# Optimization experiments

Measured on AMD Instinct MI355X. Metric: run time of the kernel, lower is better.

## Reference

```python
import jax, jax.numpy as jnp
import numpy as np

NEG_SLOPE = 0.2  # PyG GATConv default LeakyReLU slope


def _gat_conv(x, edge_index, W, a_src, a_dst, bias, heads, out_dim, concat):
    """PyG-style GATConv (eval mode, add_self_loops=True).
    x: [N, F_in], edge_index: [2, E] (row=src, col=dst)."""
    N = x.shape[0]
    loops = jnp.tile(jnp.arange(N, dtype=edge_index.dtype)[None, :], (2, 1))
    ei = jnp.concatenate([edge_index, loops], axis=1)  # [2, E+N]
    src, dst = ei[0], ei[1]

    h = (x @ W).reshape(N, heads, out_dim)            # [N, H, D]
    alpha_s = jnp.einsum('nhd,hd->nh', h, a_src)       # [N, H]
    alpha_d = jnp.einsum('nhd,hd->nh', h, a_dst)       # [N, H]

    e = jax.nn.leaky_relu(alpha_s[src] + alpha_d[dst], NEG_SLOPE)  # [E', H]
    # segment softmax over edges grouped by destination node
    m = jax.ops.segment_max(e, dst, num_segments=N)
    e = jnp.exp(e - jax.lax.stop_gradient(m)[dst])
    denom = jax.ops.segment_sum(e, dst, num_segments=N)
    alpha = e / denom[dst]                              # [E', H]

    msg = h[src] * alpha[..., None]                     # [E', H, D]
    out = jax.ops.segment_sum(msg, dst, num_segments=N) # [N, H, D]
    out = out.reshape(N, heads * out_dim) if concat else out.mean(axis=1)
    return out + bias


def setup_inputs() -> dict:
    key = jax.random.key(0)
    ks = jax.random.split(key, 12)
    N, E, F_in, H, D = 50000, 1600000, 64, 2, 32
    s = 0.1
    return {
        'x': jax.random.normal(ks[0], (N, F_in), jnp.float32),
        'edge_index': jax.random.randint(ks[1], (2, E), 0, N, jnp.int64 if jax.config.jax_enable_x64 else jnp.int32),
        'W1': jax.random.normal(ks[2], (F_in, H * D), jnp.float32) * s,
        'a_src1': jax.random.normal(ks[3], (H, D), jnp.float32) * s,
        'a_dst1': jax.random.normal(ks[4], (H, D), jnp.float32) * s,
        'b1': jnp.zeros((H * D,), jnp.float32),
        'W2': jax.random.normal(ks[5], (H * D, D), jnp.float32) * s,
        'a_src2': jax.random.normal(ks[6], (1, D), jnp.float32) * s,
        'a_dst2': jax.random.normal(ks[7], (1, D), jnp.float32) * s,
        'b2': jnp.zeros((D,), jnp.float32),
        'fcW': jax.random.normal(ks[8], (D, 1), jnp.float32) * s,
        'fcb': jnp.zeros((1,), jnp.float32),
    }


def reference(x, edge_index, W1, a_src1, a_dst1, b1, W2, a_src2, a_dst2, b2, fcW, fcb):
    H, D = 2, 32
    h = _gat_conv(x, edge_index, W1, a_src1, a_dst1, b1, heads=H, out_dim=D, concat=True)
    h = jax.nn.elu(h)
    # dropout p=0.1 is a no-op in eval mode
    h = _gat_conv(h, edge_index, W2, a_src2, a_dst2, b2, heads=1, out_dim=D, concat=False)
    h = jax.nn.elu(h)
    scores = h @ fcW + fcb
    return (scores, h)
```

## Files before the change

kernel.cpp:

```cpp
#include <hip/hip_runtime.h>
#include <hip/hip_fp16.h>

#define NEG_SLOPE 0.2f
#define NRANGE 4
#define ILV 13
#define CAP 96

__device__ __forceinline__ float elu_f(float x) {
    return x > 0.f ? x : __expf(x) - 1.f;
}
__device__ __forceinline__ float lrelu_f(float x) {
    return fmaxf(x, NEG_SLOPE * x);
}

union H4 { float2 f2; __half2 h2[2]; };

__global__ __launch_bounds__(256) void scat_gemm1_kernel(
    const int* __restrict__ ei, int* __restrict__ cnt,
    unsigned short* __restrict__ srclist, int E, int N,
    int nScat, int nChunks,
    const float* __restrict__ x, const float* __restrict__ W1,
    const float* __restrict__ a_src, const float* __restrict__ a_dst,
    __half* __restrict__ h1, float* __restrict__ as1, float* __restrict__ ad1)
{
    __shared__ float Xl[4][64];
    int b = blockIdx.x;
    if (b < ILV * nScat && (b % ILV) == 0) {
        int hid = b / ILV;
        int range = hid & (NRANGE - 1);
        int chunk = hid >> 2;
        int RS = (N + NRANGE - 1) / NRANGE;
        int lo = range * RS;
        unsigned span = (unsigned)(((lo + RS) > N ? N : (lo + RS)) - lo);
        int per = (((E + nChunks - 1) / nChunks) + 7) & ~7;
        int beg = chunk * per;
        int end = beg + per; if (end > E) end = E;
        if (beg >= E) return;

        int nfull = (end - beg) >> 11;
        for (int j = 0; j < nfull; ++j) {
            int i = beg + (j << 11) + (int)threadIdx.x * 8;
            int4 d0 = *(const int4*)(ei + E + i);
            int4 d1 = *(const int4*)(ei + E + i + 4);
            int4 s0 = *(const int4*)(ei + i);
            int4 s1 = *(const int4*)(ei + i + 4);
            int ds[8] = { d0.x, d0.y, d0.z, d0.w, d1.x, d1.y, d1.z, d1.w };
            int ss[8] = { s0.x, s0.y, s0.z, s0.w, s1.x, s1.y, s1.z, s1.w };
            int pos[8];
            bool pr[8];
#pragma unroll
            for (int k = 0; k < 8; ++k) {
                pr[k] = (unsigned)(ds[k] - lo) < span;
                if (pr[k]) pos[k] = atomicAdd(&cnt[ds[k]], 1);
            }
#pragma unroll
            for (int k = 0; k < 8; ++k) {
                if (pr[k])
                    srclist[(size_t)ds[k] * CAP + pos[k]] =
                        (unsigned short)ss[k];
            }
        }
        for (int i = beg + (nfull << 11) + (int)threadIdx.x; i < end; i += 256) {
            int dst = ei[E + i];
            if ((unsigned)(dst - lo) < span) {
                int src = ei[i];
                int pos = atomicAdd(&cnt[dst], 1);
                srclist[(size_t)dst * CAP + pos] = (unsigned short)src;
            }
        }
        return;
    }
    int gid = (b < ILV * nScat) ? (b - b / ILV - 1) : (b - nScat);
    int tid = threadIdx.x;
    int r   = tid >> 6;
    int col = tid & 63;
    int row = gid * 4 + r;
    if (row < N) Xl[r][col] = x[(size_t)row * 64 + col];
    __syncthreads();
    if (row >= N) return;

    float acc = 0.f;
#pragma unroll
    for (int k = 0; k < 64; ++k) acc += Xl[r][k] * W1[k * 64 + col];
    h1[(size_t)row * 64 + col] = __float2half(acc);

    int head = col >> 5;
    float ps = acc * a_src[col];
    float pd = acc * a_dst[col];
#pragma unroll
    for (int off = 16; off; off >>= 1) {
        ps += __shfl_xor(ps, off, 32);
        pd += __shfl_xor(pd, off, 32);
    }
    if ((col & 31) == 0) {
        as1[row * 2 + head] = ps;
        ad1[row * 2 + head] = pd;
    }
}

__global__ __launch_bounds__(256) void agg1_gemm2_kernel(
    const int* __restrict__ dcnt, const unsigned short* __restrict__ srclist,
    const __half* __restrict__ h1, const float* __restrict__ as1,
    const float* __restrict__ ad1, const float* __restrict__ b1,
    const float* __restrict__ W2, const float* __restrict__ a_s2,
    const float* __restrict__ a_d2,
    __half* __restrict__ h2, float* __restrict__ as2, float* __restrict__ ad2,
    int N)
{
    __shared__ float W2l[64 * 32];
    __shared__ float sh[4][64];
    int tid = threadIdx.x;
    for (int i = tid; i < 64 * 32; i += 256) W2l[i] = W2[i];
    __syncthreads();

    int n = (blockIdx.x * 256 + tid) >> 6;
    int lane = tid & 63;
    int wid = tid >> 6;
    if (n >= N) return;

    int grp = lane >> 4;
    int cl  = lane & 15;
    int head = cl >> 3;
    const __half* h1q = h1 + 4 * cl;
    float2 adp = *(const float2*)(ad1 + (size_t)n * 2);

    float den0 = 0.f, den1 = 0.f;
    float a0 = 0.f, a1 = 0.f, a2 = 0.f, a3 = 0.f;
    int beg = n * CAP;
    int deg = dcnt[n];
    int total = deg + 1;

    for (int base = 0; base < total; base += 64) {
        int li = base + lane;
        int es = (li < deg) ? (int)srclist[beg + li] : n;
        float2 asp = *(const float2*)(as1 + (size_t)es * 2);
        float w0 = 0.f, w1 = 0.f;
        if (li < total) {
            w0 = __expf(lrelu_f(asp.x + adp.x));
            w1 = __expf(lrelu_f(asp.y + adp.y));
        }
        den0 += w0; den1 += w1;

        int cnt = total - base; if (cnt > 64) cnt = 64;
        for (int j = 0; j < cnt; j += 16) {
            int e0 = j + grp, e1 = j + 4 + grp, e2 = j + 8 + grp, e3 = j + 12 + grp;
            int sA = __shfl(es, e0, 64);
            int sB = __shfl(es, e1, 64);
            int sC = __shfl(es, e2, 64);
            int sD = __shfl(es, e3, 64);
            float wA0 = __shfl(w0, e0, 64), wA1 = __shfl(w1, e0, 64);
            float wB0 = __shfl(w0, e1, 64), wB1 = __shfl(w1, e1, 64);
            float wC0 = __shfl(w0, e2, 64), wC1 = __shfl(w1, e2, 64);
            float wD0 = __shfl(w0, e3, 64), wD1 = __shfl(w1, e3, 64);
            float wA = head ? wA1 : wA0;
            float wB = head ? wB1 : wB0;
            float wC = head ? wC1 : wC0;
            float wD = head ? wD1 : wD0;
            H4 uA, uB, uC, uD;
            uA.f2 = *(const float2*)(h1q + (size_t)sA * 64);
            uB.f2 = *(const float2*)(h1q + (size_t)sB * 64);
            uC.f2 = *(const float2*)(h1q + (size_t)sC * 64);
            uD.f2 = *(const float2*)(h1q + (size_t)sD * 64);
            float2 gA01 = __half22float2(uA.h2[0]);
            float2 gA23 = __half22float2(uA.h2[1]);
            float2 gB01 = __half22float2(uB.h2[0]);
            float2 gB23 = __half22float2(uB.h2[1]);
            float2 gC01 = __half22float2(uC.h2[0]);
            float2 gC23 = __half22float2(uC.h2[1]);
            float2 gD01 = __half22float2(uD.h2[0]);
            float2 gD23 = __half22float2(uD.h2[1]);
            a0 += wA * gA01.x + wB * gB01.x + wC * gC01.x + wD * gD01.x;
            a1 += wA * gA01.y + wB * gB01.y + wC * gC01.y + wD * gD01.y;
            a2 += wA * gA23.x + wB * gB23.x + wC * gC23.x + wD * gD23.x;
            a3 += wA * gA23.y + wB * gB23.y + wC * gC23.y + wD * gD23.y;
        }
    }
    a0 += __shfl_xor(a0, 16, 64); a1 += __shfl_xor(a1, 16, 64);
    a2 += __shfl_xor(a2, 16, 64); a3 += __shfl_xor(a3, 16, 64);
    a0 += __shfl_xor(a0, 32, 64); a1 += __shfl_xor(a1, 32, 64);
    a2 += __shfl_xor(a2, 32, 64); a3 += __shfl_xor(a3, 32, 64);
#pragma unroll
    for (int off = 1; off < 64; off <<= 1) {
        den0 += __shfl_xor(den0, off, 64);
        den1 += __shfl_xor(den1, off, 64);
    }
    float den = head ? den1 : den0;

    float4 bb = *(const float4*)(b1 + 4 * cl);
    float inv = 1.f / den;
    float v0 = elu_f(a0 * inv + bb.x);
    float v1 = elu_f(a1 * inv + bb.y);
    float v2 = elu_f(a2 * inv + bb.z);
    float v3 = elu_f(a3 * inv + bb.w);
    if (grp == 0) ((float4*)sh[wid])[cl] = make_float4(v0, v1, v2, v3);

    int col = lane & 31;
    int kbase = (lane >> 5) * 32;
    float p = 0.f;
#pragma unroll
    for (int jj = 0; jj < 32; ++jj)
        p += sh[wid][kbase + jj] * W2l[(kbase + jj) * 32 + col];
    p += __shfl_xor(p, 32, 64);

    if (lane < 32) h2[(size_t)n * 32 + lane] = __float2half(p);

    float ps = p * a_s2[col];
    float pd = p * a_d2[col];
#pragma unroll
    for (int off = 16; off; off >>= 1) {
        ps += __shfl_xor(ps, off, 32);
        pd += __shfl_xor(pd, off, 32);
    }
    if (lane == 0) { as2[n] = ps; ad2[n] = pd; }
}

__global__ __launch_bounds__(256) void agg2_kernel(
    const int* __restrict__ dcnt, const unsigned short* __restrict__ srclist,
    const __half* __restrict__ h2, const float* __restrict__ as2,
    const float* __restrict__ ad2, const float* __restrict__ b2,
    const float* __restrict__ fcW, const float* __restrict__ fcb,
    float* __restrict__ out, int N)
{
    int g = blockIdx.x * 256 + threadIdx.x;
    int n = g >> 5;
    if (n >= N) return;
    int l32 = g & 31;
    int grp = l32 >> 3;
    int cl  = l32 & 7;
    float adn = ad2[n];
    const __half* h2q = h2 + 4 * cl;

    float denp = 0.f, a0 = 0.f, a1 = 0.f, a2 = 0.f, a3 = 0.f;
    int beg = n * CAP;
    int deg = dcnt[n];
    int total = deg + 1;

    for (int base = 0; base < total; base += 32) {
        int li = base + l32;
        int es = (li < deg) ? (int)srclist[beg + li] : n;
        float asv = as2[es];
        float w = 0.f;
        if (li < total) w = __expf(lrelu_f(asv + adn));
        denp += w;

        int cnt = total - base; if (cnt > 32) cnt = 32;
        for (int j = 0; j < cnt; j += 16) {
            int e0 = j + grp, e1 = j + 4 + grp, e2 = j + 8 + grp, e3 = j + 12 + grp;
            int sA = __shfl(es, e0, 32);
            int sB = __shfl(es, e1, 32);
            int sC = __shfl(es, e2, 32);
            int sD = __shfl(es, e3, 32);
            float wA = __shfl(w, e0, 32);
            float wB = __shfl(w, e1, 32);
            float wC = __shfl(w, e2, 32);
            float wD = __shfl(w, e3, 32);
            H4 uA, uB, uC, uD;
            uA.f2 = *(const float2*)(h2q + (size_t)sA * 32);
            uB.f2 = *(const float2*)(h2q + (size_t)sB * 32);
            uC.f2 = *(const float2*)(h2q + (size_t)sC * 32);
            uD.f2 = *(const float2*)(h2q + (size_t)sD * 32);
            float2 gA01 = __half22float2(uA.h2[0]);
            float2 gA23 = __half22float2(uA.h2[1]);
            float2 gB01 = __half22float2(uB.h2[0]);
            float2 gB23 = __half22float2(uB.h2[1]);
            float2 gC01 = __half22float2(uC.h2[0]);
            float2 gC23 = __half22float2(uC.h2[1]);
            float2 gD01 = __half22float2(uD.h2[0]);
            float2 gD23 = __half22float2(uD.h2[1]);
            a0 += wA * gA01.x + wB * gB01.x + wC * gC01.x + wD * gD01.x;
            a1 += wA * gA01.y + wB * gB01.y + wC * gC01.y + wD * gD01.y;
            a2 += wA * gA23.x + wB * gB23.x + wC * gC23.x + wD * gD23.x;
            a3 += wA * gA23.y + wB * gB23.y + wC * gC23.y + wD * gD23.y;
        }
    }
    a0 += __shfl_xor(a0, 8, 64);  a1 += __shfl_xor(a1, 8, 64);
    a2 += __shfl_xor(a2, 8, 64);  a3 += __shfl_xor(a3, 8, 64);
    a0 += __shfl_xor(a0, 16, 64); a1 += __shfl_xor(a1, 16, 64);
    a2 += __shfl_xor(a2, 16, 64); a3 += __shfl_xor(a3, 16, 64);
#pragma unroll
    for (int off = 1; off < 32; off <<= 1)
        denp += __shfl_xor(denp, off, 64);
    float den = denp;

    float4 bb = *(const float4*)(b2 + 4 * cl);
    float inv = 1.f / den;
    float v0 = elu_f(a0 * inv + bb.x);
    float v1 = elu_f(a1 * inv + bb.y);
    float v2 = elu_f(a2 * inv + bb.z);
    float v3 = elu_f(a3 * inv + bb.w);
    if (grp == 0)
        ((float4*)(out + (size_t)N + (size_t)n * 32))[cl] =
            make_float4(v0, v1, v2, v3);

    float4 fw = *(const float4*)(fcW + 4 * cl);
    float p = v0 * fw.x + v1 * fw.y + v2 * fw.z + v3 * fw.w;
    p += __shfl_xor(p, 1, 64);
    p += __shfl_xor(p, 2, 64);
    p += __shfl_xor(p, 4, 64);
    if (l32 == 0) out[n] = p + fcb[0];
}

extern "C" void kernel_launch(void* const* d_in, const int* in_sizes, int n_in,
                              void* d_out, int out_size, void* d_ws, size_t ws_size,
                              hipStream_t stream) {
    const float* x    = (const float*)d_in[0];
    const int*   ei   = (const int*)d_in[1];
    const float* W1   = (const float*)d_in[2];
    const float* a_s1 = (const float*)d_in[3];
    const float* a_d1 = (const float*)d_in[4];
    const float* b1   = (const float*)d_in[5];
    const float* W2   = (const float*)d_in[6];
    const float* a_s2 = (const float*)d_in[7];
    const float* a_d2 = (const float*)d_in[8];
    const float* b2   = (const float*)d_in[9];
    const float* fcW  = (const float*)d_in[10];
    const float* fcb  = (const float*)d_in[11];

    const int N = in_sizes[0] / 64;
    const int E = in_sizes[1] / 2;

    float* fws  = (float*)d_ws;
    float* as1  = fws;
    float* ad1  = as1 + (size_t)2 * N;
    float* as2  = ad1 + (size_t)2 * N;
    float* ad2  = as2 + (size_t)N;
    __half* h2  = (__half*)(ad2 + (size_t)N);
    __half* h1  = h2 + (size_t)32 * N;
    int*   cnt  = (int*)(h1 + (size_t)64 * N);
    unsigned short* srclist = (unsigned short*)(cnt + N);

    hipMemsetAsync(cnt, 0, sizeof(int) * (size_t)N, stream);

    const int nChunks = 256;
    const int nScat = nChunks * NRANGE;
    const int nG1 = (N + 3) / 4;
    int extra = nG1 - (ILV - 1) * nScat; if (extra < 0) extra = 0;
    scat_gemm1_kernel<<<ILV * nScat + extra, 256, 0, stream>>>(
        ei, cnt, srclist, E, N, nScat, nChunks, x, W1, a_s1, a_d1, h1, as1, ad1);

    agg1_gemm2_kernel<<<((size_t)N * 64 + 255) / 256, 256, 0, stream>>>(
        cnt, srclist, h1, as1, ad1, b1, W2, a_s2, a_d2, h2, as2, ad2, N);

    agg2_kernel<<<((size_t)N * 32 + 255) / 256, 256, 0, stream>>>(
        cnt, srclist, h2, as2, ad2, b2, fcW, fcb, (float*)d_out, N);
}
```

Measured before the change: 240.7 us.

## Split layer-1 aggregation into per-head passes and widen scatter ranges

The layer-1 gather/aggregate loop now processes each attention head in a separate pass, with 8 lanes per row-half and 8 edges in flight per step, instead of 16 lanes covering both heads with per-lane head selection. This removes the per-edge shuffles of both weights and the select, at the cost of issuing the edge-index shuffles twice and doing a longer cross-lane reduction. Separately, the scatter phase now splits destination nodes into 8 ranges instead of 4, with a smaller interleave factor, which changes how scatter blocks are spread among GEMM blocks.

```diff
diff --git a/kernel.cpp b/kernel.cpp
--- a/kernel.cpp
+++ b/kernel.cpp
@@ -2,8 +2,8 @@
 #include <hip/hip_fp16.h>
 
 #define NEG_SLOPE 0.2f
-#define NRANGE 4
-#define ILV 13
+#define NRANGE 8
+#define ILV 7
 #define CAP 96
 
 __device__ __forceinline__ float elu_f(float x) {
@@ -28,7 +28,7 @@
     if (b < ILV * nScat && (b % ILV) == 0) {
         int hid = b / ILV;
         int range = hid & (NRANGE - 1);
-        int chunk = hid >> 2;
+        int chunk = hid >> 3;
         int RS = (N + NRANGE - 1) / NRANGE;
         int lo = range * RS;
         unsigned span = (unsigned)(((lo + RS) > N ? N : (lo + RS)) - lo);
@@ -118,14 +118,15 @@
     int wid = tid >> 6;
     if (n >= N) return;
 
-    int grp = lane >> 4;
-    int cl  = lane & 15;
-    int head = cl >> 3;
-    const __half* h1q = h1 + 4 * cl;
+    int grp8 = lane >> 3;
+    int cl8  = lane & 7;
+    const __half* h1q0 = h1 + 4 * cl8;
+    const __half* h1q1 = h1 + 32 + 4 * cl8;
     float2 adp = *(const float2*)(ad1 + (size_t)n * 2);
 
     float den0 = 0.f, den1 = 0.f;
-    float a0 = 0.f, a1 = 0.f, a2 = 0.f, a3 = 0.f;
+    float p00 = 0.f, p01 = 0.f, p02 = 0.f, p03 = 0.f;
+    float p10 = 0.f, p11 = 0.f, p12 = 0.f, p13 = 0.f;
     int beg = n * CAP;
     int deg = dcnt[n];
     int total = deg + 1;
@@ -142,25 +143,23 @@
         den0 += w0; den1 += w1;
 
         int cnt = total - base; if (cnt > 64) cnt = 64;
-        for (int j = 0; j < cnt; j += 16) {
-            int e0 = j + grp, e1 = j + 4 + grp, e2 = j + 8 + grp, e3 = j + 12 + grp;
+
+        for (int j = 0; j < cnt; j += 32) {
+            int e0 = j + grp8, e1 = j + 8 + grp8;
+            int e2 = j + 16 + grp8, e3 = j + 24 + grp8;
             int sA = __shfl(es, e0, 64);
             int sB = __shfl(es, e1, 64);
             int sC = __shfl(es, e2, 64);
             int sD = __shfl(es, e3, 64);
-            float wA0 = __shfl(w0, e0, 64), wA1 = __shfl(w1, e0, 64);
-            float wB0 = __shfl(w0, e1, 64), wB1 = __shfl(w1, e1, 64);
-            float wC0 = __shfl(w0, e2, 64), wC1 = __shfl(w1, e2, 64);
-            float wD0 = __shfl(w0, e3, 64), wD1 = __shfl(w1, e3, 64);
-            float wA = head ? wA1 : wA0;
-            float wB = head ? wB1 : wB0;
-            float wC = head ? wC1 : wC0;
-            float wD = head ? wD1 : wD0;
+            float wA = __shfl(w0, e0, 64);
+            float wB = __shfl(w0, e1, 64);
+            float wC = __shfl(w0, e2, 64);
+            float wD = __shfl(w0, e3, 64);
             H4 uA, uB, uC, uD;
-            uA.f2 = *(const float2*)(h1q + (size_t)sA * 64);
-            uB.f2 = *(const float2*)(h1q + (size_t)sB * 64);
-            uC.f2 = *(const float2*)(h1q + (size_t)sC * 64);
-            uD.f2 = *(const float2*)(h1q + (size_t)sD * 64);
+            uA.f2 = *(const float2*)(h1q0 + (size_t)sA * 64);
+            uB.f2 = *(const float2*)(h1q0 + (size_t)sB * 64);
+            uC.f2 = *(const float2*)(h1q0 + (size_t)sC * 64);
+            uD.f2 = *(const float2*)(h1q0 + (size_t)sD * 64);
             float2 gA01 = __half22float2(uA.h2[0]);
             float2 gA23 = __half22float2(uA.h2[1]);
             float2 gB01 = __half22float2(uB.h2[0]);
@@ -169,30 +168,66 @@
             float2 gC23 = __half22float2(uC.h2[1]);
             float2 gD01 = __half22float2(uD.h2[0]);
             float2 gD23 = __half22float2(uD.h2[1]);
-            a0 += wA * gA01.x + wB * gB01.x + wC * gC01.x + wD * gD01.x;
-            a1 += wA * gA01.y + wB * gB01.y + wC * gC01.y + wD * gD01.y;
-            a2 += wA * gA23.x + wB * gB23.x + wC * gC23.x + wD * gD23.x;
-            a3 += wA * gA23.y + wB * gB23.y + wC * gC23.y + wD * gD23.y;
-        }
-    }
-    a0 += __shfl_xor(a0, 16, 64); a1 += __shfl_xor(a1, 16, 64);
-    a2 += __shfl_xor(a2, 16, 64); a3 += __shfl_xor(a3, 16, 64);
-    a0 += __shfl_xor(a0, 32, 64); a1 += __shfl_xor(a1, 32, 64);
-    a2 += __shfl_xor(a2, 32, 64); a3 += __shfl_xor(a3, 32, 64);
+            p00 += wA * gA01.x + wB * gB01.x + wC * gC01.x + wD * gD01.x;
+            p01 += wA * gA01.y + wB * gB01.y + wC * gC01.y + wD * gD01.y;
+            p02 += wA * gA23.x + wB * gB23.x + wC * gC23.x + wD * gD23.x;
+            p03 += wA * gA23.y + wB * gB23.y + wC * gC23.y + wD * gD23.y;
+        }
+        for (int j = 0; j < cnt; j += 32) {
+            int e0 = j + grp8, e1 = j + 8 + grp8;
+            int e2 = j + 16 + grp8, e3 = j + 24 + grp8;
+            int sA = __shfl(es, e0, 64);
+            int sB = __shfl(es, e1, 64);
+            int sC = __shfl(es, e2, 64);
+            int sD = __shfl(es, e3, 64);
+            float wA = __shfl(w1, e0, 64);
+            float wB = __shfl(w1, e1, 64);
+            float wC = __shfl(w1, e2, 64);
+            float wD = __shfl(w1, e3, 64);
+            H4 uA, uB, uC, uD;
+            uA.f2 = *(const float2*)(h1q1 + (size_t)sA * 64);
+            uB.f2 = *(const float2*)(h1q1 + (size_t)sB * 64);
+            uC.f2 = *(const float2*)(h1q1 + (size_t)sC * 64);
+            uD.f2 = *(const float2*)(h1q1 + (size_t)sD * 64);
+            float2 gA01 = __half22float2(uA.h2[0]);
+            float2 gA23 = __half22float2(uA.h2[1]);
+            float2 gB01 = __half22float2(uB.h2[0]);
+            float2 gB23 = __half22float2(uB.h2[1]);
+            float2 gC01 = __half22float2(uC.h2[0]);
+            float2 gC23 = __half22float2(uC.h2[1]);
+            float2 gD01 = __half22float2(uD.h2[0]);
+            float2 gD23 = __half22float2(uD.h2[1]);
+            p10 += wA * gA01.x + wB * gB01.x + wC * gC01.x + wD * gD01.x;
+            p11 += wA * gA01.y + wB * gB01.y + wC * gC01.y + wD * gD01.y;
+            p12 += wA * gA23.x + wB * gB23.x + wC * gC23.x + wD * gD23.x;
+            p13 += wA * gA23.y + wB * gB23.y + wC * gC23.y + wD * gD23.y;
+        }
+    }
+#pragma unroll
+    for (int off = 8; off < 64; off <<= 1) {
+        p00 += __shfl_xor(p00, off, 64); p01 += __shfl_xor(p01, off, 64);
+        p02 += __shfl_xor(p02, off, 64); p03 += __shfl_xor(p03, off, 64);
+        p10 += __shfl_xor(p10, off, 64); p11 += __shfl_xor(p11, off, 64);
+        p12 += __shfl_xor(p12, off, 64); p13 += __shfl_xor(p13, off, 64);
+    }
 #pragma unroll
     for (int off = 1; off < 64; off <<= 1) {
         den0 += __shfl_xor(den0, off, 64);
         den1 += __shfl_xor(den1, off, 64);
     }
-    float den = head ? den1 : den0;
-
-    float4 bb = *(const float4*)(b1 + 4 * cl);
-    float inv = 1.f / den;
-    float v0 = elu_f(a0 * inv + bb.x);
-    float v1 = elu_f(a1 * inv + bb.y);
-    float v2 = elu_f(a2 * inv + bb.z);
-    float v3 = elu_f(a3 * inv + bb.w);
-    if (grp == 0) ((float4*)sh[wid])[cl] = make_float4(v0, v1, v2, v3);
+
+    if (grp8 == 0) {
+        float inv0 = 1.f / den0;
+        float inv1 = 1.f / den1;
+        float4 bb0 = *(const float4*)(b1 + 4 * cl8);
+        float4 bb1 = *(const float4*)(b1 + 32 + 4 * cl8);
+        ((float4*)sh[wid])[cl8] = make_float4(
+            elu_f(p00 * inv0 + bb0.x), elu_f(p01 * inv0 + bb0.y),
+            elu_f(p02 * inv0 + bb0.z), elu_f(p03 * inv0 + bb0.w));
+        ((float4*)sh[wid])[8 + cl8] = make_float4(
+            elu_f(p10 * inv1 + bb1.x), elu_f(p11 * inv1 + bb1.y),
+            elu_f(p12 * inv1 + bb1.z), elu_f(p13 * inv1 + bb1.w));
+    }
 
     int col = lane & 31;
     int kbase = (lane >> 5) * 32;
```

After: 246.1 us. +2.2%, slower.
